# Kernel optimization log

Hardware: AMD Instinct MI355X
Metric: run time of the kernel (lower is better)

The kernel has to match this reference:

```python
import jax, jax.numpy as jnp
import numpy as np

EPS = 1e-5
K = 20

def knn_idx(x, k):
    # x: (B, N, C) -> (B, N, k) indices of k nearest neighbors (negative sq-dist top-k, self included)
    sq = jnp.sum(x * x, axis=-1)                      # (B, N)
    inner = jnp.einsum('bnc,bmc->bnm', x, x)          # (B, N, N)
    neg_dist = 2.0 * inner - sq[:, :, None] - sq[:, None, :]
    _, idx = jax.lax.top_k(neg_dist, k)
    return idx

def edge_conv(x, w, g, b, m, v, k):
    # x: (B, N, C); w: (O, 2C); BN eval-mode params over O
    idx = knn_idx(x, k)                               # (B, N, k)
    nb = jax.vmap(lambda f, i: f[i])(x, idx)          # (B, N, k, C)
    ctr = x[:, :, None, :]
    e = jnp.concatenate([nb - ctr, jnp.broadcast_to(ctr, nb.shape)], axis=-1)  # (B,N,k,2C)
    h = jnp.einsum('bnkc,oc->bnko', e, w)
    h = (h - m) * jax.lax.rsqrt(v + EPS) * g + b
    h = jnp.where(h > 0, h, 0.2 * h)                  # LeakyReLU(0.2)
    return jnp.max(h, axis=2)                         # (B, N, O)

def conv1d_bn_relu(x, w, bias, g, bt, m, v):
    h = jnp.einsum('bnc,oc->bno', x, w) + bias
    h = (h - m) * jax.lax.rsqrt(v + EPS) * g + bt
    return jax.nn.relu(h)

def setup_inputs() -> dict:
    key = jax.random.key(0)
    ks = jax.random.split(key, 16)
    B, N = 2, 4096
    d = {'x': jax.random.normal(ks[0], (B, N, 3), dtype=jnp.float32)}
    dims = [(3, 64), (64, 64), (64, 128), (128, 256)]
    for i, (ci, co) in enumerate(dims, start=1):
        d[f'w{i}'] = jax.random.normal(ks[i], (co, 2 * ci), dtype=jnp.float32) * 0.05
        d[f'g{i}'] = jnp.ones((co,), jnp.float32)
        d[f'bt{i}'] = jnp.zeros((co,), jnp.float32)
        d[f'm{i}'] = jnp.zeros((co,), jnp.float32)
        d[f'v{i}'] = jnp.ones((co,), jnp.float32)
    head = [(512, 256), (256, 128)]
    for i, (ci, co) in enumerate(head, start=1):
        d[f'hw{i}'] = jax.random.normal(ks[8 + i], (co, ci), dtype=jnp.float32) * 0.05
        d[f'hb{i}'] = jnp.zeros((co,), jnp.float32)
        d[f'hg{i}'] = jnp.ones((co,), jnp.float32)
        d[f'hbt{i}'] = jnp.zeros((co,), jnp.float32)
        d[f'hm{i}'] = jnp.zeros((co,), jnp.float32)
        d[f'hv{i}'] = jnp.ones((co,), jnp.float32)
    d['hw3'] = jax.random.normal(ks[12], (1, 128), dtype=jnp.float32) * 0.05
    d['hb3'] = jnp.zeros((1,), jnp.float32)
    return d

def reference(x, w1, g1, bt1, m1, v1, w2, g2, bt2, m2, v2, w3, g3, bt3, m3, v3,
              w4, g4, bt4, m4, v4,
              hw1, hb1, hg1, hbt1, hm1, hv1, hw2, hb2, hg2, hbt2, hm2, hv2, hw3, hb3):
    x1 = edge_conv(x, w1, g1, bt1, m1, v1, K)   # (B, N, 64)
    x2 = edge_conv(x1, w2, g2, bt2, m2, v2, K)  # (B, N, 64)
    x3 = edge_conv(x2, w3, g3, bt3, m3, v3, K)  # (B, N, 128)
    x4 = edge_conv(x3, w4, g4, bt4, m4, v4, K)  # (B, N, 256)
    xc = jnp.concatenate([x1, x2, x3, x4], axis=-1)  # (B, N, 512)
    h = conv1d_bn_relu(xc, hw1, hb1, hg1, hbt1, hm1, hv1)
    h = conv1d_bn_relu(h, hw2, hb2, hg2, hbt2, hm2, hv2)
    out = jnp.einsum('bnc,oc->bno', h, hw3) + hb3    # (B, N, 1)
    return out[..., 0]                               # (B, N)
```

## Files before the change

### kernel.cpp

```cpp
#include <hip/hip_runtime.h>

#define NPTS 4096
#define EPSF 1e-5f

__device__ __forceinline__ unsigned f2u(float f) {
  unsigned b = __float_as_uint(f);
  return (b & 0x80000000u) ? ~b : (b | 0x80000000u);
}
__device__ __forceinline__ float u2f(unsigned u) {
  unsigned b = (u & 0x80000000u) ? (u & 0x7fffffffu) : ~u;
  return __uint_as_float(b);
}
__device__ __forceinline__ unsigned shflx(unsigned v, int j) {
  return (unsigned)__shfl_xor((int)v, j);
}
__device__ __forceinline__ unsigned long long shflx64(unsigned long long v, int j) {
  unsigned lo = (unsigned)__shfl_xor((int)(unsigned)(v & 0xffffffffull), j);
  unsigned hi = (unsigned)__shfl_xor((int)(unsigned)(v >> 32), j);
  return ((unsigned long long)hi << 32) | lo;
}

__device__ __forceinline__ unsigned sort64_u32(unsigned v, int lane) {
#pragma unroll
  for (int k = 2; k <= 64; k <<= 1) {
#pragma unroll
    for (int j = k >> 1; j >= 1; j >>= 1) {
      unsigned ov = shflx(v, j);
      bool kmin = ((lane & j) == 0) == ((lane & k) == 0);
      v = kmin ? (v < ov ? v : ov) : (v > ov ? v : ov);
    }
  }
  return v;
}

__device__ __forceinline__ void sort128_u32(unsigned& a, unsigned& b, int lane) {
#pragma unroll
  for (int k = 2; k <= 128; k <<= 1) {
#pragma unroll
    for (int j = k >> 1; j >= 1; j >>= 1) {
      if (j == 64) {
        unsigned mn = a < b ? a : b, mx = a < b ? b : a;
        a = mn; b = mx;
      } else {
        unsigned oa = shflx(a, j), ob = shflx(b, j);
        bool lower = (lane & j) == 0;
        bool asca, ascb;
        if (k == 128) { asca = true; ascb = true; }
        else if (k == 64) { asca = true; ascb = false; }
        else { asca = ((lane & k) == 0); ascb = asca; }
        a = (lower == asca) ? (a < oa ? a : oa) : (a > oa ? a : oa);
        b = (lower == ascb) ? (b < ob ? b : ob) : (b > ob ? b : ob);
      }
    }
  }
}

__device__ __forceinline__ unsigned long long sort64_u64(unsigned long long v, int lane) {
#pragma unroll
  for (int k = 2; k <= 64; k <<= 1) {
#pragma unroll
    for (int j = k >> 1; j >= 1; j >>= 1) {
      unsigned long long ov = shflx64(v, j);
      bool kmin = ((lane & j) == 0) == ((lane & k) == 0);
      v = kmin ? (v < ov ? v : ov) : (v > ov ? v : ov);
    }
  }
  return v;
}

__device__ __forceinline__ void sort128_u64(unsigned long long& a, unsigned long long& b,
                                            int lane) {
#pragma unroll
  for (int k = 2; k <= 128; k <<= 1) {
#pragma unroll
    for (int j = k >> 1; j >= 1; j >>= 1) {
      if (j == 64) {
        unsigned long long mn = a < b ? a : b, mx = a < b ? b : a;
        a = mn; b = mx;
      } else {
        unsigned long long oa = shflx64(a, j), ob = shflx64(b, j);
        bool lower = (lane & j) == 0;
        bool asca, ascb;
        if (k == 128) { asca = true; ascb = true; }
        else if (k == 64) { asca = true; ascb = false; }
        else { asca = ((lane & k) == 0); ascb = asca; }
        a = (lower == asca) ? (a < oa ? a : oa) : (a > oa ? a : oa);
        b = (lower == ascb) ? (b < ob ? b : ob) : (b > ob ? b : ob);
      }
    }
  }
}

struct TopkShared {
  unsigned wv[80];
  unsigned ck[128];
  int      ci[128];
  int      cnt_s;
  int      selm[20];
  float    part[4 * 256];
  float    fcv[80];
  int      fcm[80];
};

template <int MAP>
__device__ __forceinline__ int tk_enc(int j, int tid) {
  if (MAP == 0) return j * 256 + tid;
  return ((j >> 2) << 10) | (tid << 2) | (j & 3);
}

template <int MAP>
__device__ __forceinline__ void topk_select(float v[16], TopkShared& sh,
                                            int tid, int lane, int wid) {
  float M = v[0];
#pragma unroll
  for (int j = 1; j < 16; ++j) M = fmaxf(M, v[j]);

  unsigned mk = sort64_u32(f2u(M), lane);

  if (tid == 0) sh.cnt_s = 0;
  if (lane >= 44) sh.wv[wid * 20 + (63 - lane)] = mk;
  __syncthreads();

  unsigned a0 = sh.wv[lane];
  unsigned b0 = (lane < 16) ? sh.wv[64 + lane] : 0u;
  sort128_u32(a0, b0, lane);
  unsigned T0k = (unsigned)__shfl((int)b0, 44);
  float T0f = u2f(T0k);

#pragma unroll
  for (int j = 0; j < 16; ++j) {
    bool pred = (v[j] >= T0f);
    unsigned long long m = __ballot(pred);
    int below = __popcll(m & ((1ull << lane) - 1ull));
    int cw = __popcll(m);
    int base = 0;
    if (lane == 0 && cw) base = atomicAdd(&sh.cnt_s, cw);
    base = __shfl(base, 0);
    if (pred) {
      int pos = base + below;
      if (pos < 128) { sh.ck[pos] = f2u(v[j]); sh.ci[pos] = tk_enc<MAP>(j, tid); }
    }
  }
  __syncthreads();
  const int cnt = sh.cnt_s;

  if (cnt <= 128) {
    if (wid == 0) {
      unsigned long long k0 = (lane < cnt)
          ? (((unsigned long long)sh.ck[lane] << 32) | (unsigned)(~sh.ci[lane])) : 0ull;
      if (cnt <= 64) {
        k0 = sort64_u64(k0, lane);
        if (lane >= 44) sh.selm[63 - lane] = (int)(~(unsigned)k0);
      } else {
        unsigned long long k1 = (64 + lane < cnt)
            ? (((unsigned long long)sh.ck[64 + lane] << 32) | (unsigned)(~sh.ci[64 + lane]))
            : 0ull;
        sort128_u64(k0, k1, lane);
        if (lane >= 44) sh.selm[63 - lane] = (int)(~(unsigned)k1);
      }
    }
  } else {
    for (int it = 0; it < 20; ++it) {
      float bv = v[0]; int bj = 0;
#pragma unroll
      for (int j = 1; j < 16; ++j)
        if (v[j] > bv) { bv = v[j]; bj = j; }
      int bm = tk_enc<MAP>(bj, tid);
#pragma unroll
      for (int off = 1; off < 64; off <<= 1) {
        float ov = __shfl_xor(bv, off);
        int om = __shfl_xor(bm, off);
        if (ov > bv || (ov == bv && om < bm)) { bv = ov; bm = om; }
      }
      if (lane == 0) { sh.fcv[wid * 20 + it] = bv; sh.fcm[wid * 20 + it] = bm; }
      if (MAP == 0) {
        if ((bm & 255) == tid) v[bm >> 8] = -3.0e38f;
      } else {
        if (((bm >> 2) & 255) == tid) v[(((bm >> 10) & 3) << 2) | (bm & 3)] = -3.0e38f;
      }
    }
    __syncthreads();
    if (wid == 0) {
      float c0 = sh.fcv[lane]; int m0 = sh.fcm[lane];
      float c1 = (lane < 16) ? sh.fcv[64 + lane] : -3.0e38f;
      int   m1 = (lane < 16) ? sh.fcm[64 + lane] : 0x7fffffff;
      for (int it = 0; it < 20; ++it) {
        float bv; int bm, bs;
        if (c0 > c1 || (c0 == c1 && m0 < m1)) { bv = c0; bm = m0; bs = lane; }
        else { bv = c1; bm = m1; bs = 64 + lane; }
#pragma unroll
        for (int off = 1; off < 64; off <<= 1) {
          float ov = __shfl_xor(bv, off);
          int om = __shfl_xor(bm, off);
          int os = __shfl_xor(bs, off);
          if (ov > bv || (ov == bv && om < bm)) { bv = ov; bm = om; bs = os; }
        }
        if (lane == 0) sh.selm[it] = bm;
        if (bs == lane) c0 = -3.0e38f;
        else if (bs == 64 + lane) c1 = -3.0e38f;
      }
    }
  }
  __syncthreads();
}

__device__ __forceinline__ void topk_gather(const TopkShared& sh, TopkShared& shm,
                                            const float* __restrict__ P,
                                            const float* __restrict__ Q,
                                            float* __restrict__ Y, int ldy, int O,
                                            int bBase, int n, int tid, int lane, int wid) {
  for (int o = lane; o < O; o += 64) {
    float q = Q[(size_t)(bBase + n) * O + o];
    float best = -3.0e38f;
#pragma unroll
    for (int kk = 0; kk < 5; ++kk) {
      int s = sh.selm[wid * 5 + kk];
      float t = P[(size_t)(bBase + s) * O + o] + q;
      t = t > 0.f ? t : 0.2f * t;
      best = fmaxf(best, t);
    }
    shm.part[wid * 256 + o] = best;
  }
  __syncthreads();
  for (int o = tid; o < O; o += 256) {
    float b2 = fmaxf(fmaxf(shm.part[o], shm.part[256 + o]),
                     fmaxf(shm.part[512 + o], shm.part[768 + o]));
    Y[(size_t)(bBase + n) * ldy + o] = b2;
  }
}

__global__ void fold_edge_k(const float* __restrict__ w, const float* __restrict__ g,
                            const float* __restrict__ bt, const float* __restrict__ m,
                            const float* __restrict__ v, int O, int C,
                            float* __restrict__ wdf, float* __restrict__ wqf,
                            float* __restrict__ c0) {
  int t = blockIdx.x * 256 + threadIdx.x;
  if (t >= O * C) return;
  int o = t / C, c = t - o * C;
  float A = g[o] * (1.0f / sqrtf(v[o] + EPSF));
  float wd = w[o * 2 * C + c], wc = w[o * 2 * C + C + c];
  wdf[t] = A * wd;
  wqf[t] = A * (wc - wd);
  if (c == 0) c0[o] = bt[o] - m[o] * A;
}

__global__ void fold_head_k(const float* __restrict__ hw, const float* __restrict__ hb,
                            const float* __restrict__ hg, const float* __restrict__ hbt,
                            const float* __restrict__ hm, const float* __restrict__ hv,
                            int O, int C, float* __restrict__ hwf, float* __restrict__ cb) {
  int t = blockIdx.x * 256 + threadIdx.x;
  if (t >= O * C) return;
  int o = t / C, c = t - o * C;
  float A = hg[o] * (1.0f / sqrtf(hv[o] + EPSF));
  hwf[t] = A * hw[t];
  if (c == 0) cb[o] = (hb[o] - hm[o]) * A + hbt[o];
}

__global__ void sq_k(const float* __restrict__ X, int lda, int C,
                     float* __restrict__ sq, int nrows) {
  int r = blockIdx.x * 256 + threadIdx.x;
  if (r >= nrows) return;
  const float* p = X + (size_t)r * lda;
  float s = 0.f;
  for (int c = 0; c < C; ++c) s += p[c] * p[c];
  sq[r] = s;
}

__global__ void pq3_k(const float* __restrict__ x, const float* __restrict__ wdf,
                      const float* __restrict__ wqf, const float* __restrict__ c0,
                      float* __restrict__ P, float* __restrict__ Q) {
  int t = blockIdx.x * 256 + threadIdx.x;
  int r = t >> 6, o = t & 63;
  float x0 = x[r * 3], x1 = x[r * 3 + 1], x2 = x[r * 3 + 2];
  P[(size_t)r * 64 + o] = x0 * wdf[o * 3] + x1 * wdf[o * 3 + 1] + x2 * wdf[o * 3 + 2];
  Q[(size_t)r * 64 + o] = x0 * wqf[o * 3] + x1 * wqf[o * 3 + 1] + x2 * wqf[o * 3 + 2] + c0[o];
}

__global__ __launch_bounds__(256) void topk_l1_fused(
    const float* __restrict__ x, const float* __restrict__ sqg,
    const float* __restrict__ P, const float* __restrict__ Q,
    float* __restrict__ Y, int ldy) {
  const int tid = threadIdx.x;
  const int lane = tid & 63, wid = tid >> 6;
  const int n = blockIdx.x;
  const int bBase = blockIdx.y * NPTS;
  const float* xb = x + (size_t)bBase * 3;
  const float* sqb = sqg + bBase;

  __shared__ TopkShared sh;

  float xn0 = xb[n * 3], xn1 = xb[n * 3 + 1], xn2 = xb[n * 3 + 2];
  float sn = sqb[n];
  float v[16];
#pragma unroll
  for (int j = 0; j < 16; ++j) {
    int mc = j * 256 + tid;
    float y0 = xb[mc * 3], y1 = xb[mc * 3 + 1], y2 = xb[mc * 3 + 2];
    float inner = xn0 * y0 + xn1 * y1 + xn2 * y2;
    v[j] = 2.0f * inner - sn - sqb[mc];
  }

  topk_select<0>(v, sh, tid, lane, wid);
  topk_gather(sh, sh, P, Q, Y, ldy, 64, bBase, n, tid, lane, wid);
}

__global__ __launch_bounds__(256) void dist_sym64_k(
    const float* __restrict__ X0, int lda, int C,
    const float* __restrict__ sq0, float* __restrict__ D0) {
  int t = blockIdx.x;
  int bi = 0;
  while (t >= 64 - bi) { t -= 64 - bi; ++bi; }
  const int bj = bi + t;
  const int b = blockIdx.y;
  const float* X = X0 + (size_t)b * NPTS * lda;
  const float* sq = sq0 + (size_t)b * NPTS;
  float* D = D0 + (size_t)b * NPTS * NPTS;

  const int row0 = bi * 64, col0 = bj * 64;
  const int tid = threadIdx.x;
  const int tx = tid & 15, ty = tid >> 4;

  __shared__ __align__(16) float As[16][68];
  __shared__ __align__(16) float Bs[16][68];

  const int lr = tid >> 2;
  const int lc = (tid & 3) << 2;
  const float* Ap = X + (size_t)(row0 + lr) * lda + lc;
  const float* Bp = X + (size_t)(col0 + lr) * lda + lc;

  float acc[4][4] = {};
  for (int c0 = 0; c0 < C; c0 += 16) {
    float4 av = *(const float4*)(Ap + c0);
    float4 bv = *(const float4*)(Bp + c0);
    As[lc + 0][lr] = av.x; As[lc + 1][lr] = av.y;
    As[lc + 2][lr] = av.z; As[lc + 3][lr] = av.w;
    Bs[lc + 0][lr] = bv.x; Bs[lc + 1][lr] = bv.y;
    Bs[lc + 2][lr] = bv.z; Bs[lc + 3][lr] = bv.w;
    __syncthreads();
#pragma unroll
    for (int c = 0; c < 16; ++c) {
      float4 a4 = *(const float4*)(&As[c][ty << 2]);
      float4 b4 = *(const float4*)(&Bs[c][tx << 2]);
      float aa[4] = {a4.x, a4.y, a4.z, a4.w};
      float bb[4] = {b4.x, b4.y, b4.z, b4.w};
#pragma unroll
      for (int i = 0; i < 4; ++i)
#pragma unroll
        for (int j = 0; j < 4; ++j) acc[i][j] = fmaf(aa[i], bb[j], acc[i][j]);
    }
    __syncthreads();
  }

  float rs[4], cs[4];
#pragma unroll
  for (int i = 0; i < 4; ++i) rs[i] = sq[row0 + (ty << 2) + i];
#pragma unroll
  for (int j = 0; j < 4; ++j) cs[j] = sq[col0 + (tx << 2) + j];

#pragma unroll
  for (int i = 0; i < 4; ++i) {
    const int row = row0 + (ty << 2) + i;
    float vals[4];
#pragma unroll
    for (int j = 0; j < 4; ++j) vals[j] = (2.0f * acc[i][j] - rs[i]) - cs[j];
    *(float4*)&D[(size_t)row * NPTS + col0 + (tx << 2)] =
        make_float4(vals[0], vals[1], vals[2], vals[3]);
  }

  if (bi != bj) {
#pragma unroll
    for (int j = 0; j < 4; ++j) {
      const int col = col0 + (tx << 2) + j;
      float mv[4];
#pragma unroll
      for (int i = 0; i < 4; ++i) mv[i] = (2.0f * acc[i][j] - cs[j]) - rs[i];
      *(float4*)&D[(size_t)col * NPTS + row0 + (ty << 2)] =
          make_float4(mv[0], mv[1], mv[2], mv[3]);
    }
  }
}

__global__ __launch_bounds__(256) void gemm_pq(
    const float* __restrict__ A, int lda,
    const float* __restrict__ Wd, const float* __restrict__ Wq, int ldb,
    float* __restrict__ P, float* __restrict__ Q, int ldo, int C,
    const float* __restrict__ c0b) {
  __shared__ __align__(16) float As[16][68];
  __shared__ __align__(16) float Bd[16][68];
  __shared__ __align__(16) float Bq[16][68];
  const int tx = threadIdx.x, ty = threadIdx.y;
  const int tid = ty * 16 + tx;
  const int row0 = blockIdx.y * 64, col0 = blockIdx.x * 64;
  const int lr = tid >> 2;
  const int lc = (tid & 3) << 2;
  const float* Ap = A + (size_t)(row0 + lr) * lda + lc;
  const float* Dp = Wd + (size_t)(col0 + lr) * ldb + lc;
  const float* Qp = Wq + (size_t)(col0 + lr) * ldb + lc;
  float accp[4][4] = {};
  float accq[4][4] = {};
  for (int c0 = 0; c0 < C; c0 += 16) {
    float4 av = *(const float4*)(Ap + c0);
    float4 dv = *(const float4*)(Dp + c0);
    float4 qv = *(const float4*)(Qp + c0);
    As[lc + 0][lr] = av.x; As[lc + 1][lr] = av.y;
    As[lc + 2][lr] = av.z; As[lc + 3][lr] = av.w;
    Bd[lc + 0][lr] = dv.x; Bd[lc + 1][lr] = dv.y;
    Bd[lc + 2][lr] = dv.z; Bd[lc + 3][lr] = dv.w;
    Bq[lc + 0][lr] = qv.x; Bq[lc + 1][lr] = qv.y;
    Bq[lc + 2][lr] = qv.z; Bq[lc + 3][lr] = qv.w;
    __syncthreads();
#pragma unroll
    for (int c = 0; c < 16; ++c) {
      float4 a4 = *(const float4*)(&As[c][ty << 2]);
      float4 d4 = *(const float4*)(&Bd[c][tx << 2]);
      float4 q4 = *(const float4*)(&Bq[c][tx << 2]);
      float aa[4] = {a4.x, a4.y, a4.z, a4.w};
      float dd[4] = {d4.x, d4.y, d4.z, d4.w};
      float qq[4] = {q4.x, q4.y, q4.z, q4.w};
#pragma unroll
      for (int i = 0; i < 4; ++i)
#pragma unroll
        for (int j = 0; j < 4; ++j) {
          accp[i][j] = fmaf(aa[i], dd[j], accp[i][j]);
          accq[i][j] = fmaf(aa[i], qq[j], accq[i][j]);
        }
    }
    __syncthreads();
  }
  const int row = row0 + (ty << 2), col = col0 + (tx << 2);
#pragma unroll
  for (int i = 0; i < 4; ++i) {
    *(float4*)(&P[(size_t)(row + i) * ldo + col]) = make_float4(
        accp[i][0], accp[i][1], accp[i][2], accp[i][3]);
    *(float4*)(&Q[(size_t)(row + i) * ldo + col]) = make_float4(
        accq[i][0] + c0b[col + 0], accq[i][1] + c0b[col + 1],
        accq[i][2] + c0b[col + 2], accq[i][3] + c0b[col + 3]);
  }
}

template <int EPI>
__global__ __launch_bounds__(256) void gemm_nt(
    const float* __restrict__ A, int lda,
    const float* __restrict__ Bm, int ldb,
    float* __restrict__ Out, int ldo, int C,
    const float* __restrict__ sqA, const float* __restrict__ sqB,
    const float* __restrict__ bias) {
  __shared__ __align__(16) float As[16][68];
  __shared__ __align__(16) float Bs[16][68];
  const int tx = threadIdx.x, ty = threadIdx.y;
  const int tid = ty * 16 + tx;
  const int row0 = blockIdx.y * 64, col0 = blockIdx.x * 64;
  const int lr = tid >> 2;
  const int lc = (tid & 3) << 2;
  const float* Ap = A + (size_t)(row0 + lr) * lda + lc;
  const float* Bp = Bm + (size_t)(col0 + lr) * ldb + lc;
  float acc[4][4] = {};
  for (int c0 = 0; c0 < C; c0 += 16) {
    float4 av = *(const float4*)(Ap + c0);
    float4 bv = *(const float4*)(Bp + c0);
    As[lc + 0][lr] = av.x; As[lc + 1][lr] = av.y;
    As[lc + 2][lr] = av.z; As[lc + 3][lr] = av.w;
    Bs[lc + 0][lr] = bv.x; Bs[lc + 1][lr] = bv.y;
    Bs[lc + 2][lr] = bv.z; Bs[lc + 3][lr] = bv.w;
    __syncthreads();
#pragma unroll
    for (int c = 0; c < 16; ++c) {
      float4 a4 = *(const float4*)(&As[c][ty << 2]);
      float4 b4 = *(const float4*)(&Bs[c][tx << 2]);
      float aa[4] = {a4.x, a4.y, a4.z, a4.w};
      float bb[4] = {b4.x, b4.y, b4.z, b4.w};
#pragma unroll
      for (int i = 0; i < 4; ++i)
#pragma unroll
        for (int j = 0; j < 4; ++j) acc[i][j] = fmaf(aa[i], bb[j], acc[i][j]);
    }
    __syncthreads();
  }
  const int row = row0 + (ty << 2), col = col0 + (tx << 2);
#pragma unroll
  for (int i = 0; i < 4; ++i) {
    float vals[4];
#pragma unroll
    for (int j = 0; j < 4; ++j) {
      float va = acc[i][j];
      if (EPI == 0) vals[j] = va;
      else if (EPI == 1) vals[j] = va + bias[col + j];
      else if (EPI == 2) vals[j] = 2.0f * va - sqA[row + i] - sqB[col + j];
      else { float t = va + bias[col + j]; vals[j] = t > 0.f ? t : 0.f; }
    }
    *(float4*)(&Out[(size_t)(row + i) * ldo + col]) =
        make_float4(vals[0], vals[1], vals[2], vals[3]);
  }
}

__global__ __launch_bounds__(256) void topk_max_f32(
    const float* __restrict__ D, long long dStride,
    const float* __restrict__ P, const float* __restrict__ Q,
    float* __restrict__ Y, int ldy, int O, int bBase0, int r0) {
  const int tid = threadIdx.x;
  const int lane = tid & 63, wid = tid >> 6;
  const int nloc = blockIdx.x;
  const int n = r0 + nloc;
  const int bBase = bBase0 + blockIdx.y * NPTS;
  const float* drow = D + (size_t)blockIdx.y * (size_t)dStride + (size_t)nloc * NPTS;

  __shared__ TopkShared sh;

  float v[16];
#pragma unroll
  for (int c = 0; c < 4; ++c) {
    float4 f = *(const float4*)&drow[c * 1024 + tid * 4];
    v[c * 4 + 0] = f.x; v[c * 4 + 1] = f.y;
    v[c * 4 + 2] = f.z; v[c * 4 + 3] = f.w;
  }

  topk_select<1>(v, sh, tid, lane, wid);
  topk_gather(sh, sh, P, Q, Y, ldy, O, bBase, n, tid, lane, wid);
}

__global__ void final_dot_k(const float* __restrict__ h2, const float* __restrict__ w3,
                            const float* __restrict__ b3, float* __restrict__ out) {
  int gt = blockIdx.x * 256 + threadIdx.x;
  int row = gt >> 6, lane = gt & 63;
  float s = h2[(size_t)row * 128 + lane] * w3[lane] +
            h2[(size_t)row * 128 + 64 + lane] * w3[64 + lane];
#pragma unroll
  for (int off = 32; off > 0; off >>= 1) s += __shfl_down(s, off);
  if (lane == 0) out[row] = s + b3[0];
}

extern "C" void kernel_launch(void* const* d_in, const int* in_sizes, int n_in,
                              void* d_out, int out_size, void* d_ws, size_t ws_size,
                              hipStream_t stream) {
  const int B = 2, N = NPTS;
  const size_t NN = (size_t)N * N;
  const float* x = (const float*)d_in[0];
  const float* w[4]  = {(const float*)d_in[1], (const float*)d_in[6],
                        (const float*)d_in[11], (const float*)d_in[16]};
  const float* g[4]  = {(const float*)d_in[2], (const float*)d_in[7],
                        (const float*)d_in[12], (const float*)d_in[17]};
  const float* bt[4] = {(const float*)d_in[3], (const float*)d_in[8],
                        (const float*)d_in[13], (const float*)d_in[18]};
  const float* mm[4] = {(const float*)d_in[4], (const float*)d_in[9],
                        (const float*)d_in[14], (const float*)d_in[19]};
  const float* vv[4] = {(const float*)d_in[5], (const float*)d_in[10],
                        (const float*)d_in[15], (const float*)d_in[20]};
  const float* hw1 = (const float*)d_in[21]; const float* hb1 = (const float*)d_in[22];
  const float* hg1 = (const float*)d_in[23]; const float* hbt1 = (const float*)d_in[24];
  const float* hm1 = (const float*)d_in[25]; const float* hv1 = (const float*)d_in[26];
  const float* hw2 = (const float*)d_in[27]; const float* hb2 = (const float*)d_in[28];
  const float* hg2 = (const float*)d_in[29]; const float* hbt2 = (const float*)d_in[30];
  const float* hm2 = (const float*)d_in[31]; const float* hv2 = (const float*)d_in[32];
  const float* hw3 = (const float*)d_in[33]; const float* hb3 = (const float*)d_in[34];
  float* out = (float*)d_out;

  char* wsb = (char*)d_ws;
  size_t off = 0;
  auto alloc = [&](size_t nbytes) {
    char* p = wsb + off;
    off += (nbytes + 255) & ~(size_t)255;
    return p;
  };
  float* xc   = (float*)alloc((size_t)B * N * 512 * 4);
  float* P    = (float*)alloc((size_t)B * N * 256 * 4);
  float* Q    = (float*)alloc((size_t)B * N * 256 * 4);
  float* sq   = (float*)alloc((size_t)B * N * 4);
  float* wdf  = (float*)alloc(256 * 256 * 4);
  float* wqf  = (float*)alloc(256 * 256 * 4);
  float* c0   = (float*)alloc(256 * 4);
  float* hwf1 = (float*)alloc(256 * 512 * 4);
  float* cb1  = (float*)alloc(256 * 4);
  float* hwf2 = (float*)alloc(128 * 256 * 4);
  float* cb2  = (float*)alloc(128 * 4);
  float* D    = (float*)(wsb + off);
  size_t avail = (ws_size > off) ? (ws_size - off) : 0;
  const bool merged = (avail >= (size_t)B * NN * 4);
  int rows_tile = 4096;
  if (!merged)
    while ((size_t)rows_tile * N * 4 > avail && rows_tile > 64) rows_tile >>= 1;

  const int Cin[4]  = {3, 64, 64, 128};
  const int Oc[4]   = {64, 64, 128, 256};
  const int ioff[4] = {0, 0, 64, 128};
  const int ooff[4] = {0, 64, 128, 256};
  dim3 blk2(16, 16);

  for (int L = 0; L < 4; ++L) {
    const int C = Cin[L], O = Oc[L];
    const float* in = (L == 0) ? x : (xc + ioff[L]);
    const int lda = (L == 0) ? 3 : 512;

    fold_edge_k<<<dim3((O * C + 255) / 256), dim3(256), 0, stream>>>(
        w[L], g[L], bt[L], mm[L], vv[L], O, C, wdf, wqf, c0);
    sq_k<<<dim3((B * N + 255) / 256), dim3(256), 0, stream>>>(in, lda, C, sq, B * N);
    if (L == 0) {
      pq3_k<<<dim3(B * N * 64 / 256), dim3(256), 0, stream>>>(x, wdf, wqf, c0, P, Q);
    } else {
      gemm_pq<<<dim3(O / 64, B * N / 64), blk2, 0, stream>>>(
          in, lda, wdf, wqf, C, P, Q, O, C, c0);
    }

    if (L == 0) {
      topk_l1_fused<<<dim3(N, B), dim3(256), 0, stream>>>(
          x, sq, P, Q, xc + ooff[0], 512);
      continue;
    }
    if (merged) {
      dist_sym64_k<<<dim3(2080, B), dim3(256), 0, stream>>>(in, lda, C, sq, D);
      topk_max_f32<<<dim3(N, B), dim3(256), 0, stream>>>(
          D, (long long)NN, P, Q, xc + ooff[L], 512, O, 0, 0);
      continue;
    }
    for (int b = 0; b < B; ++b) {
      for (int r0 = 0; r0 < N; r0 += rows_tile) {
        gemm_nt<2><<<dim3(N / 64, rows_tile / 64), blk2, 0, stream>>>(
            in + ((size_t)b * N + r0) * lda, lda, in + (size_t)b * N * lda, lda,
            D, N, C, sq + b * N + r0, sq + b * N, nullptr);
        topk_max_f32<<<dim3(rows_tile, 1), dim3(256), 0, stream>>>(
            D, 0, P, Q, xc + ooff[L], 512, O, b * N, r0);
      }
    }
  }

  fold_head_k<<<dim3((256 * 512 + 255) / 256), dim3(256), 0, stream>>>(
      hw1, hb1, hg1, hbt1, hm1, hv1, 256, 512, hwf1, cb1);
  fold_head_k<<<dim3((128 * 256 + 255) / 256), dim3(256), 0, stream>>>(
      hw2, hb2, hg2, hbt2, hm2, hv2, 128, 256, hwf2, cb2);

  float* h1 = P;
  float* h2 = Q;
  gemm_nt<3><<<dim3(256 / 64, B * N / 64), blk2, 0, stream>>>(
      xc, 512, hwf1, 512, h1, 256, 512, nullptr, nullptr, cb1);
  gemm_nt<3><<<dim3(128 / 64, B * N / 64), blk2, 0, stream>>>(
      h1, 256, hwf2, 256, h2, 128, 256, nullptr, nullptr, cb2);
  final_dot_k<<<dim3(B * N / 4), dim3(256), 0, stream>>>(h2, hw3, hb3, out);
}
```

Before: 609.4 us.

## Overlap batch-1 distance tiles with batch-0 top-k in a fused launch

```diff
diff --git a/kernel.cpp b/kernel.cpp
--- a/kernel.cpp
+++ b/kernel.cpp
@@ -229,6 +229,89 @@
   }
 }
 
+__device__ __forceinline__ void topk_row_body(
+    const float* __restrict__ drow, TopkShared& sh,
+    const float* __restrict__ P, const float* __restrict__ Q,
+    float* __restrict__ Y, int ldy, int O, int bBase, int n,
+    int tid, int lane, int wid) {
+  float v[16];
+#pragma unroll
+  for (int c = 0; c < 4; ++c) {
+    float4 f = *(const float4*)&drow[c * 1024 + tid * 4];
+    v[c * 4 + 0] = f.x; v[c * 4 + 1] = f.y;
+    v[c * 4 + 2] = f.z; v[c * 4 + 3] = f.w;
+  }
+  topk_select<1>(v, sh, tid, lane, wid);
+  topk_gather(sh, sh, P, Q, Y, ldy, O, bBase, n, tid, lane, wid);
+}
+
+__device__ __forceinline__ void dist_tile_body(
+    int t, const float* __restrict__ X, int lda, int C,
+    const float* __restrict__ sq, float* __restrict__ D,
+    float As[16][68], float Bs[16][68], int tid) {
+  int bi = 0;
+  while (t >= 64 - bi) { t -= 64 - bi; ++bi; }
+  const int bj = bi + t;
+  const int row0 = bi * 64, col0 = bj * 64;
+  const int tx = tid & 15, ty = tid >> 4;
+
+  const int lr = tid >> 2;
+  const int lc = (tid & 3) << 2;
+  const float* Ap = X + (size_t)(row0 + lr) * lda + lc;
+  const float* Bp = X + (size_t)(col0 + lr) * lda + lc;
+
+  float acc[4][4] = {};
+  for (int c0 = 0; c0 < C; c0 += 16) {
+    float4 av = *(const float4*)(Ap + c0);
+    float4 bv = *(const float4*)(Bp + c0);
+    As[lc + 0][lr] = av.x; As[lc + 1][lr] = av.y;
+    As[lc + 2][lr] = av.z; As[lc + 3][lr] = av.w;
+    Bs[lc + 0][lr] = bv.x; Bs[lc + 1][lr] = bv.y;
+    Bs[lc + 2][lr] = bv.z; Bs[lc + 3][lr] = bv.w;
+    __syncthreads();
+#pragma unroll
+    for (int c = 0; c < 16; ++c) {
+      float4 a4 = *(const float4*)(&As[c][ty << 2]);
+      float4 b4 = *(const float4*)(&Bs[c][tx << 2]);
+      float aa[4] = {a4.x, a4.y, a4.z, a4.w};
+      float bb[4] = {b4.x, b4.y, b4.z, b4.w};
+#pragma unroll
+      for (int i = 0; i < 4; ++i)
+#pragma unroll
+        for (int j = 0; j < 4; ++j) acc[i][j] = fmaf(aa[i], bb[j], acc[i][j]);
+    }
+    __syncthreads();
+  }
+
+  float rs[4], cs[4];
+#pragma unroll
+  for (int i = 0; i < 4; ++i) rs[i] = sq[row0 + (ty << 2) + i];
+#pragma unroll
+  for (int j = 0; j < 4; ++j) cs[j] = sq[col0 + (tx << 2) + j];
+
+#pragma unroll
+  for (int i = 0; i < 4; ++i) {
+    const int row = row0 + (ty << 2) + i;
+    float vals[4];
+#pragma unroll
+    for (int j = 0; j < 4; ++j) vals[j] = (2.0f * acc[i][j] - rs[i]) - cs[j];
+    *(float4*)&D[(size_t)row * NPTS + col0 + (tx << 2)] =
+        make_float4(vals[0], vals[1], vals[2], vals[3]);
+  }
+
+  if (bi != bj) {
+#pragma unroll
+    for (int j = 0; j < 4; ++j) {
+      const int col = col0 + (tx << 2) + j;
+      float mv[4];
+#pragma unroll
+      for (int i = 0; i < 4; ++i) mv[i] = (2.0f * acc[i][j] - cs[j]) - rs[i];
+      *(float4*)&D[(size_t)col * NPTS + row0 + (ty << 2)] =
+          make_float4(mv[0], mv[1], mv[2], mv[3]);
+    }
+  }
+}
+
 __global__ void fold_edge_k(const float* __restrict__ w, const float* __restrict__ g,
                             const float* __restrict__ bt, const float* __restrict__ m,
                             const float* __restrict__ v, int O, int C,
@@ -307,76 +390,32 @@
 __global__ __launch_bounds__(256) void dist_sym64_k(
     const float* __restrict__ X0, int lda, int C,
     const float* __restrict__ sq0, float* __restrict__ D0) {
-  int t = blockIdx.x;
-  int bi = 0;
-  while (t >= 64 - bi) { t -= 64 - bi; ++bi; }
-  const int bj = bi + t;
   const int b = blockIdx.y;
-  const float* X = X0 + (size_t)b * NPTS * lda;
-  const float* sq = sq0 + (size_t)b * NPTS;
-  float* D = D0 + (size_t)b * NPTS * NPTS;
-
-  const int row0 = bi * 64, col0 = bj * 64;
-  const int tid = threadIdx.x;
-  const int tx = tid & 15, ty = tid >> 4;
-
   __shared__ __align__(16) float As[16][68];
   __shared__ __align__(16) float Bs[16][68];
-
-  const int lr = tid >> 2;
-  const int lc = (tid & 3) << 2;
-  const float* Ap = X + (size_t)(row0 + lr) * lda + lc;
-  const float* Bp = X + (size_t)(col0 + lr) * lda + lc;
-
-  float acc[4][4] = {};
-  for (int c0 = 0; c0 < C; c0 += 16) {
-    float4 av = *(const float4*)(Ap + c0);
-    float4 bv = *(const float4*)(Bp + c0);
-    As[lc + 0][lr] = av.x; As[lc + 1][lr] = av.y;
-    As[lc + 2][lr] = av.z; As[lc + 3][lr] = av.w;
-    Bs[lc + 0][lr] = bv.x; Bs[lc + 1][lr] = bv.y;
-    Bs[lc + 2][lr] = bv.z; Bs[lc + 3][lr] = bv.w;
-    __syncthreads();
-#pragma unroll
-    for (int c = 0; c < 16; ++c) {
-      float4 a4 = *(const float4*)(&As[c][ty << 2]);
-      float4 b4 = *(const float4*)(&Bs[c][tx << 2]);
-      float aa[4] = {a4.x, a4.y, a4.z, a4.w};
-      float bb[4] = {b4.x, b4.y, b4.z, b4.w};
-#pragma unroll
-      for (int i = 0; i < 4; ++i)
-#pragma unroll
-        for (int j = 0; j < 4; ++j) acc[i][j] = fmaf(aa[i], bb[j], acc[i][j]);
-    }
-    __syncthreads();
-  }
-
-  float rs[4], cs[4];
-#pragma unroll
-  for (int i = 0; i < 4; ++i) rs[i] = sq[row0 + (ty << 2) + i];
-#pragma unroll
-  for (int j = 0; j < 4; ++j) cs[j] = sq[col0 + (tx << 2) + j];
-
-#pragma unroll
-  for (int i = 0; i < 4; ++i) {
-    const int row = row0 + (ty << 2) + i;
-    float vals[4];
-#pragma unroll
-    for (int j = 0; j < 4; ++j) vals[j] = (2.0f * acc[i][j] - rs[i]) - cs[j];
-    *(float4*)&D[(size_t)row * NPTS + col0 + (tx << 2)] =
-        make_float4(vals[0], vals[1], vals[2], vals[3]);
-  }
-
-  if (bi != bj) {
-#pragma unroll
-    for (int j = 0; j < 4; ++j) {
-      const int col = col0 + (tx << 2) + j;
-      float mv[4];
-#pragma unroll
-      for (int i = 0; i < 4; ++i) mv[i] = (2.0f * acc[i][j] - cs[j]) - rs[i];
-      *(float4*)&D[(size_t)col * NPTS + row0 + (ty << 2)] =
-          make_float4(mv[0], mv[1], mv[2], mv[3]);
-    }
+  dist_tile_body(blockIdx.x, X0 + (size_t)b * NPTS * lda, lda, C,
+                 sq0 + (size_t)b * NPTS, D0 + (size_t)b * NPTS * NPTS,
+                 As, Bs, threadIdx.x);
+}
+
+__global__ __launch_bounds__(256) void dist_topk_fused(
+    const float* __restrict__ X1, int lda, int C,
+    const float* __restrict__ sq1, float* __restrict__ D1,
+    const float* __restrict__ D0,
+    const float* __restrict__ P, const float* __restrict__ Q,
+    float* __restrict__ Y, int ldy, int O, int bBase0) {
+  __shared__ union {
+    struct { float As[16][68]; float Bs[16][68]; } g;
+    TopkShared t;
+  } u;
+  const int tid = threadIdx.x;
+  if (blockIdx.x < 2080) {
+    dist_tile_body(blockIdx.x, X1, lda, C, sq1, D1, u.g.As, u.g.Bs, tid);
+  } else {
+    const int n = blockIdx.x - 2080;
+    const int lane = tid & 63, wid = tid >> 6;
+    topk_row_body(D0 + (size_t)n * NPTS, u.t, P, Q, Y, ldy, O, bBase0, n,
+                  tid, lane, wid);
   }
 }
 
@@ -503,19 +542,8 @@
   const int n = r0 + nloc;
   const int bBase = bBase0 + blockIdx.y * NPTS;
   const float* drow = D + (size_t)blockIdx.y * (size_t)dStride + (size_t)nloc * NPTS;
-
   __shared__ TopkShared sh;
-
-  float v[16];
-#pragma unroll
-  for (int c = 0; c < 4; ++c) {
-    float4 f = *(const float4*)&drow[c * 1024 + tid * 4];
-    v[c * 4 + 0] = f.x; v[c * 4 + 1] = f.y;
-    v[c * 4 + 2] = f.z; v[c * 4 + 3] = f.w;
-  }
-
-  topk_select<1>(v, sh, tid, lane, wid);
-  topk_gather(sh, sh, P, Q, Y, ldy, O, bBase, n, tid, lane, wid);
+  topk_row_body(drow, sh, P, Q, Y, ldy, O, bBase, n, tid, lane, wid);
 }
 
 __global__ void final_dot_k(const float* __restrict__ h2, const float* __restrict__ w3,
@@ -606,9 +634,12 @@
       continue;
     }
     if (merged) {
-      dist_sym64_k<<<dim3(2080, B), dim3(256), 0, stream>>>(in, lda, C, sq, D);
-      topk_max_f32<<<dim3(N, B), dim3(256), 0, stream>>>(
-          D, (long long)NN, P, Q, xc + ooff[L], 512, O, 0, 0);
+      dist_sym64_k<<<dim3(2080, 1), dim3(256), 0, stream>>>(in, lda, C, sq, D);
+      dist_topk_fused<<<dim3(2080 + 4096), dim3(256), 0, stream>>>(
+          in + (size_t)N * lda, lda, C, sq + N, D + NN,
+          D, P, Q, xc + ooff[L], 512, O, 0);
+      topk_max_f32<<<dim3(N, 1), dim3(256), 0, stream>>>(
+          D + NN, 0, P, Q, xc + ooff[L], 512, O, N, 0);
       continue;
     }
     for (int b = 0; b < B; ++b) {
```

Result: slower. 665.0 us (+9.1%).

## Prune top-k search using per-64-column block maxima from distance kernel

Applied to the files above, without the earlier changes.

```diff
diff --git a/kernel.cpp b/kernel.cpp
--- a/kernel.cpp
+++ b/kernel.cpp
@@ -100,6 +100,9 @@
   float    part[4 * 256];
   float    fcv[80];
   int      fcm[80];
+  int      sblk[64];
+  int      nsel;
+  unsigned tkey;
 };
 
 template <int MAP>
@@ -306,7 +309,8 @@
 
 __global__ __launch_bounds__(256) void dist_sym64_k(
     const float* __restrict__ X0, int lda, int C,
-    const float* __restrict__ sq0, float* __restrict__ D0) {
+    const float* __restrict__ sq0, float* __restrict__ D0,
+    float* __restrict__ M0) {
   int t = blockIdx.x;
   int bi = 0;
   while (t >= 64 - bi) { t -= 64 - bi; ++bi; }
@@ -315,6 +319,7 @@
   const float* X = X0 + (size_t)b * NPTS * lda;
   const float* sq = sq0 + (size_t)b * NPTS;
   float* D = D0 + (size_t)b * NPTS * NPTS;
+  float* M = M0 + (size_t)b * NPTS * 64;
 
   const int row0 = bi * 64, col0 = bj * 64;
   const int tid = threadIdx.x;
@@ -365,9 +370,16 @@
     for (int j = 0; j < 4; ++j) vals[j] = (2.0f * acc[i][j] - rs[i]) - cs[j];
     *(float4*)&D[(size_t)row * NPTS + col0 + (tx << 2)] =
         make_float4(vals[0], vals[1], vals[2], vals[3]);
+    float rm = fmaxf(fmaxf(vals[0], vals[1]), fmaxf(vals[2], vals[3]));
+    rm = fmaxf(rm, __shfl_xor(rm, 1));
+    rm = fmaxf(rm, __shfl_xor(rm, 2));
+    rm = fmaxf(rm, __shfl_xor(rm, 4));
+    rm = fmaxf(rm, __shfl_xor(rm, 8));
+    if (tx == 0) M[(size_t)row * 64 + bj] = rm;
   }
 
   if (bi != bj) {
+    float cm4[4];
 #pragma unroll
     for (int j = 0; j < 4; ++j) {
       const int col = col0 + (tx << 2) + j;
@@ -376,7 +388,17 @@
       for (int i = 0; i < 4; ++i) mv[i] = (2.0f * acc[i][j] - cs[j]) - rs[i];
       *(float4*)&D[(size_t)col * NPTS + row0 + (ty << 2)] =
           make_float4(mv[0], mv[1], mv[2], mv[3]);
-    }
+      cm4[j] = fmaxf(fmaxf(mv[0], mv[1]), fmaxf(mv[2], mv[3]));
+    }
+#pragma unroll
+    for (int j = 0; j < 4; ++j) As[ty][(tx << 2) + j] = cm4[j];
+    __syncthreads();
+    const int colq = tid >> 2, q = tid & 3;
+    float m = fmaxf(fmaxf(As[q * 4 + 0][colq], As[q * 4 + 1][colq]),
+                    fmaxf(As[q * 4 + 2][colq], As[q * 4 + 3][colq]));
+    m = fmaxf(m, __shfl_xor(m, 1));
+    m = fmaxf(m, __shfl_xor(m, 2));
+    if (q == 0) M[(size_t)(col0 + colq) * 64 + bi] = m;
   }
 }
 
@@ -493,6 +515,90 @@
   }
 }
 
+__global__ __launch_bounds__(256) void topk_blkmax(
+    const float* __restrict__ D, long long dStride, const float* __restrict__ Mg,
+    const float* __restrict__ P, const float* __restrict__ Q,
+    float* __restrict__ Y, int ldy, int O) {
+  const int tid = threadIdx.x;
+  const int lane = tid & 63, wid = tid >> 6;
+  const int n = blockIdx.x;
+  const int b = blockIdx.y;
+  const int bBase = b * NPTS;
+  const float* drow = D + (size_t)b * (size_t)dStride + (size_t)n * NPTS;
+  const float* mrow = Mg + ((size_t)(bBase + n)) * 64;
+
+  __shared__ TopkShared sh;
+
+  if (tid == 0) sh.cnt_s = 0;
+  if (wid == 0) {
+    float mval = mrow[lane];
+    unsigned key = sort64_u32(f2u(mval), lane);
+    unsigned tk = (unsigned)__shfl((int)key, 44);
+    bool pred = (f2u(mval) >= tk);
+    unsigned long long bm = __ballot(pred);
+    int pos = (int)__popcll(bm & ((1ull << lane) - 1ull));
+    if (pred) sh.sblk[pos] = lane;
+    if (lane == 0) { sh.nsel = (int)__popcll(bm); sh.tkey = tk; }
+  }
+  __syncthreads();
+  const int ns = sh.nsel;
+  const float Tvf = u2f(sh.tkey);
+
+  for (int c0 = 0; c0 < ns; c0 += 4) {
+    int bidx = c0 + wid;
+    bool act = (bidx < ns);
+    float v = -3.0e38f;
+    int gcol = 0;
+    if (act) {
+      int blk = sh.sblk[bidx];
+      gcol = (blk << 6) + lane;
+      v = drow[gcol];
+    }
+    bool pred = act && (v >= Tvf);
+    unsigned long long m = __ballot(pred);
+    int below = (int)__popcll(m & ((1ull << lane) - 1ull));
+    int cw = (int)__popcll(m);
+    int base = 0;
+    if (lane == 0 && cw) base = atomicAdd(&sh.cnt_s, cw);
+    base = __shfl(base, 0);
+    if (pred) {
+      int pos = base + below;
+      if (pos < 128) { sh.ck[pos] = f2u(v); sh.ci[pos] = gcol; }
+    }
+  }
+  __syncthreads();
+  const int cnt = sh.cnt_s;
+
+  if (cnt <= 128) {
+    if (wid == 0) {
+      unsigned long long k0 = (lane < cnt)
+          ? (((unsigned long long)sh.ck[lane] << 32) | (unsigned)(~sh.ci[lane])) : 0ull;
+      if (cnt <= 64) {
+        k0 = sort64_u64(k0, lane);
+        if (lane >= 44) sh.selm[63 - lane] = (int)(~(unsigned)k0);
+      } else {
+        unsigned long long k1 = (64 + lane < cnt)
+            ? (((unsigned long long)sh.ck[64 + lane] << 32) | (unsigned)(~sh.ci[64 + lane]))
+            : 0ull;
+        sort128_u64(k0, k1, lane);
+        if (lane >= 44) sh.selm[63 - lane] = (int)(~(unsigned)k1);
+      }
+    }
+    __syncthreads();
+  } else {
+    float v[16];
+#pragma unroll
+    for (int c = 0; c < 4; ++c) {
+      float4 f = *(const float4*)&drow[c * 1024 + tid * 4];
+      v[c * 4 + 0] = f.x; v[c * 4 + 1] = f.y;
+      v[c * 4 + 2] = f.z; v[c * 4 + 3] = f.w;
+    }
+    topk_select<1>(v, sh, tid, lane, wid);
+  }
+
+  topk_gather(sh, sh, P, Q, Y, ldy, O, bBase, n, tid, lane, wid);
+}
+
 __global__ __launch_bounds__(256) void topk_max_f32(
     const float* __restrict__ D, long long dStride,
     const float* __restrict__ P, const float* __restrict__ Q,
@@ -503,9 +609,7 @@
   const int n = r0 + nloc;
   const int bBase = bBase0 + blockIdx.y * NPTS;
   const float* drow = D + (size_t)blockIdx.y * (size_t)dStride + (size_t)nloc * NPTS;
-
   __shared__ TopkShared sh;
-
   float v[16];
 #pragma unroll
   for (int c = 0; c < 4; ++c) {
@@ -513,7 +617,6 @@
     v[c * 4 + 0] = f.x; v[c * 4 + 1] = f.y;
     v[c * 4 + 2] = f.z; v[c * 4 + 3] = f.w;
   }
-
   topk_select<1>(v, sh, tid, lane, wid);
   topk_gather(sh, sh, P, Q, Y, ldy, O, bBase, n, tid, lane, wid);
 }
@@ -572,6 +675,7 @@
   float* cb1  = (float*)alloc(256 * 4);
   float* hwf2 = (float*)alloc(128 * 256 * 4);
   float* cb2  = (float*)alloc(128 * 4);
+  float* Mg   = (float*)alloc((size_t)B * N * 64 * 4);
   float* D    = (float*)(wsb + off);
   size_t avail = (ws_size > off) ? (ws_size - off) : 0;
   const bool merged = (avail >= (size_t)B * NN * 4);
@@ -606,9 +710,9 @@
       continue;
     }
     if (merged) {
-      dist_sym64_k<<<dim3(2080, B), dim3(256), 0, stream>>>(in, lda, C, sq, D);
-      topk_max_f32<<<dim3(N, B), dim3(256), 0, stream>>>(
-          D, (long long)NN, P, Q, xc + ooff[L], 512, O, 0, 0);
+      dist_sym64_k<<<dim3(2080, B), dim3(256), 0, stream>>>(in, lda, C, sq, D, Mg);
+      topk_blkmax<<<dim3(N, B), dim3(256), 0, stream>>>(
+          D, (long long)NN, Mg, P, Q, xc + ooff[L], 512, O);
       continue;
     }
     for (int b = 0; b < B; ++b) {
```

New measurement: 598.7 us. About the same (-1.8%).
